# Kernel tuning notes

Measured on AMD Instinct MI355X. Metric: run time of the kernel, lower is better.

## Reference

```python
import jax, jax.numpy as jnp
import numpy as np

B, Cin, Cout, T, H, W = 8, 64, 64, 16, 32, 32
AH = 64  # attention_hidden_dims


def setup_inputs() -> dict:
    key = jax.random.key(0)
    ks = jax.random.split(key, 6)
    s = 0.05
    return {
        "X": jax.random.normal(ks[0], (B, Cin, T, H, W), jnp.float32),
        # 1x1 conv weights of the SelfAttention module (bias zero-init like nn.Conv2d default is uniform, but zeros is fine for a reference baseline)
        "q_w": jax.random.normal(ks[1], (AH, Cin), jnp.float32) * s,
        "q_b": jnp.zeros((AH,), jnp.float32),
        "k_w": jax.random.normal(ks[2], (AH, Cin), jnp.float32) * s,
        "k_b": jnp.zeros((AH,), jnp.float32),
        "v_w": jax.random.normal(ks[3], (Cin, Cin), jnp.float32) * s,
        "v_b": jnp.zeros((Cin,), jnp.float32),
        # ConvLSTM gate conv: concat([x, h]) -> 4*Cout channels, 3x3, padding 1
        "conv_w": jax.random.normal(ks[4], (4 * Cout, Cin + Cout, 3, 3), jnp.float32) * s,
        "conv_b": jnp.zeros((4 * Cout,), jnp.float32),
        # peephole weights, zero-init per WeightsInitializer.Zeros
        "w_ci": jnp.zeros((Cout, H, W), jnp.float32),
        "w_cf": jnp.zeros((Cout, H, W), jnp.float32),
        "w_co": jnp.zeros((Cout, H, W), jnp.float32),
    }


def _self_attention(x, q_w, q_b, k_w, k_b, v_w, v_b):
    # x: (B, Cin, H, W). 1x1 convs expressed as channel contractions.
    b, c, h, w = x.shape
    xf = x.reshape(b, c, h * w)                                    # (B, C, HW)
    q = jnp.einsum('oc,bcn->bno', q_w, xf) + q_b                   # (B, HW, AH)
    k = jnp.einsum('oc,bcn->bon', k_w, xf) + k_b[None, :, None]    # (B, AH, HW)
    v = jnp.einsum('oc,bcn->bon', v_w, xf) + v_b[None, :, None]    # (B, Cin, HW)
    attn = jax.nn.softmax(jnp.einsum('bno,bom->bnm', q, k), axis=-1)  # (B, HW, HW)
    out = jnp.einsum('bnm,bcm->bcn', attn, v).reshape(b, c, h, w)  # (B, Cin, H, W)
    return out, attn


def _convlstm_cell(x, h, c, conv_w, conv_b, w_ci, w_cf, w_co):
    z = jnp.concatenate([x, h], axis=1)  # (B, Cin+Cout, H, W)
    conv = jax.lax.conv_general_dilated(
        z, conv_w, window_strides=(1, 1), padding='SAME',
        dimension_numbers=('NCHW', 'OIHW', 'NCHW')) + conv_b[None, :, None, None]
    i_c, f_c, g_c, o_c = jnp.split(conv, 4, axis=1)
    i = jax.nn.sigmoid(i_c + w_ci * c)
    f = jax.nn.sigmoid(f_c + w_cf * c)
    new_c = f * c + i * jnp.tanh(g_c)
    o = jax.nn.sigmoid(o_c + w_co * new_c)
    new_h = o * jnp.tanh(new_c)
    return new_h, new_c


def reference(X, q_w, q_b, k_w, k_b, v_w, v_b, conv_w, conv_b, w_ci, w_cf, w_co):
    b = X.shape[0]
    h0 = jnp.zeros((b, Cout, H, W), X.dtype)
    c0 = jnp.zeros_like(h0)
    xs = jnp.moveaxis(X, 2, 0)  # (T, B, Cin, H, W) for scan over time

    def step(carry, x_t):
        h, c = carry
        ax, _ = _self_attention(x_t, q_w, q_b, k_w, k_b, v_w, v_b)
        new_h, new_c = _convlstm_cell(ax, h, c, conv_w, conv_b, w_ci, w_cf, w_co)
        return (new_h, new_c), new_h

    _, hs = jax.lax.scan(step, (h0, c0), xs)  # hs: (T, B, Cout, H, W)
    return jnp.moveaxis(hs, 0, 2)  # (B, Cout, T, H, W)
```

## Files before the change

### kernel.cpp

```cpp
#include <hip/hip_runtime.h>
#include <math.h>

typedef __attribute__((ext_vector_type(8))) __bf16 bf16x8;
typedef __attribute__((ext_vector_type(4))) float f32x4;
typedef unsigned short u16;
typedef unsigned int u32;

#define MFMA16(a, b, c) __builtin_amdgcn_mfma_f32_16x16x32_bf16(a, b, c, 0, 0, 0)

__device__ __forceinline__ u16 f2bf(float f) {
    u32 u = __float_as_uint(f);
    return (u16)((u + 0x7fffu + ((u >> 16) & 1u)) >> 16);
}
__device__ __forceinline__ float bf2f(u16 h) {
    return __uint_as_float(((u32)h) << 16);
}

__global__ __launch_bounds__(256) void k_wtrans2(const float* __restrict__ cw,
                                                 u16* __restrict__ whi,
                                                 u16* __restrict__ wlo) {
    int idx = blockIdx.x * 256 + threadIdx.x;
    if (idx >= 294912) return;
    int s   = idx >> 15;
    int ocp = (idx >> 7) & 255;
    int ic  = idx & 127;
    int q = ocp >> 5, cc = (ocp >> 2) & 7, g = ocp & 3;
    int oc = g * 64 + q * 8 + cc;
    float f = cw[oc * 1152 + ic * 9 + s];
    u16 hi = f2bf(f);
    whi[idx] = hi;
    wlo[idx] = f2bf(f - bf2f(hi));
}

__global__ __launch_bounds__(256) void k_qkvw(
    const float* __restrict__ qw, const float* __restrict__ kw,
    const float* __restrict__ vw, u16* __restrict__ w2h, u16* __restrict__ w2l)
{
    int idx = blockIdx.x * 256 + threadIdx.x;
    if (idx >= 12288) return;
    int o = idx >> 6, c = idx & 63;
    float f = (o < 64) ? qw[o * 64 + c]
            : (o < 128) ? kw[(o - 64) * 64 + c]
                        : vw[(o - 128) * 64 + c];
    u16 hi = f2bf(f);
    w2h[idx] = hi;
    w2l[idx] = f2bf(f - bf2f(hi));
}

__global__ __launch_bounds__(256) void k_qkv2(
    const float* __restrict__ X,
    const u16* __restrict__ w2h, const u16* __restrict__ w2l,
    const float* __restrict__ qb, const float* __restrict__ kb,
    const float* __restrict__ vb,
    u16* __restrict__ qmat, u16* __restrict__ kmat, u16* __restrict__ vt)
{
    __shared__ u16 bhs[4096];
    __shared__ u16 bls[4096];

    const int tid = threadIdx.x;
    const int ns = blockIdx.x;
    const int bt = blockIdx.y;
    const int b = bt >> 4, t = bt & 15;
    const int n0 = ns * 64;

    const float* xb = X + (size_t)b * 1048576 + (size_t)t * 1024 + n0;
    for (int i = tid; i < 4096; i += 256) {
        int c = i >> 6, n = i & 63;
        float f = xb[(size_t)c * 16384 + n];
        u16 hi = f2bf(f);
        u16 lo = f2bf(f - bf2f(hi));
        int ci = c ^ ((n & 7) << 3);
        bhs[n * 64 + ci] = hi;
        bls[n * 64 + ci] = lo;
    }
    __syncthreads();

    const int wv = tid >> 6, lane = tid & 63;
    const int l15 = lane & 15, l4 = lane >> 4;
    const int o0 = wv * 48;

    f32x4 acc[3][4];
#pragma unroll
    for (int ot = 0; ot < 3; ++ot)
#pragma unroll
        for (int nt = 0; nt < 4; ++nt) acc[ot][nt] = (f32x4){0.f, 0.f, 0.f, 0.f};

#pragma unroll
    for (int kk = 0; kk < 2; ++kk) {
        bf16x8 Ah[3], Al[3];
#pragma unroll
        for (int ot = 0; ot < 3; ++ot) {
            int off = (o0 + ot * 16 + l15) * 64 + kk * 32 + l4 * 8;
            Ah[ot] = *reinterpret_cast<const bf16x8*>(w2h + off);
            Al[ot] = *reinterpret_cast<const bf16x8*>(w2l + off);
        }
#pragma unroll
        for (int nt = 0; nt < 4; ++nt) {
            int n = nt * 16 + l15;
            int gran = (kk * 4 + l4) ^ (n & 7);
            bf16x8 Bh = *reinterpret_cast<const bf16x8*>(bhs + n * 64 + gran * 8);
            bf16x8 Bl = *reinterpret_cast<const bf16x8*>(bls + n * 64 + gran * 8);
#pragma unroll
            for (int ot = 0; ot < 3; ++ot) {
                acc[ot][nt] = MFMA16(Ah[ot], Bh, acc[ot][nt]);
                acc[ot][nt] = MFMA16(Ah[ot], Bl, acc[ot][nt]);
                acc[ot][nt] = MFMA16(Al[ot], Bh, acc[ot][nt]);
            }
        }
    }

#pragma unroll
    for (int ot = 0; ot < 3; ++ot) {
#pragma unroll
        for (int r = 0; r < 4; ++r) {
            int row = o0 + ot * 16 + l4 * 4 + r;
            float bias = (row < 64) ? qb[row]
                       : (row < 128) ? kb[row - 64] : vb[row - 128];
#pragma unroll
            for (int nt = 0; nt < 4; ++nt) {
                int col = n0 + nt * 16 + l15;
                u16 h = f2bf(acc[ot][nt][r] + bias);
                if (row < 64)
                    qmat[(size_t)bt * 65536 + (size_t)col * 64 + row] = h;
                else if (row < 128)
                    kmat[(size_t)bt * 65536 + (size_t)col * 64 + (row - 64)] = h;
                else
                    vt[(size_t)bt * 65536 + (size_t)(row - 128) * 1024 + col] = h;
            }
        }
    }
}

__global__ __launch_bounds__(256, 4) void k_attn(
    const u16* __restrict__ qmat, const u16* __restrict__ kmat,
    const u16* __restrict__ vt, u16* __restrict__ za)
{
    __shared__ char kl[16384];
    __shared__ char vl[16384];
    __shared__ u16 plds[4 * 16 * 40];

    const int tid = threadIdx.x;
    const int id  = blockIdx.x;
    const int w   = (id & 7) * 256 + (id >> 3);
    const int bt  = w >> 4;
    const int ntile = w & 15;

    const int wv = tid >> 6, lane = tid & 63;
    const int l15 = lane & 15, l4 = lane >> 4;
    const int n0 = ntile * 64 + wv * 16;

    const u16* qb_ = qmat + (size_t)bt * 65536;
    const u16* kb_ = kmat + (size_t)bt * 65536;
    const u16* vb_ = vt + (size_t)bt * 65536;

    bf16x8 qf0 = *reinterpret_cast<const bf16x8*>(qb_ + (n0 + l15) * 64 + l4 * 8);
    bf16x8 qf1 = *reinterpret_cast<const bf16x8*>(qb_ + (n0 + l15) * 64 + 32 + l4 * 8);

    f32x4 oacc[4];
#pragma unroll
    for (int ct = 0; ct < 4; ++ct) oacc[ct] = (f32x4){0.f, 0.f, 0.f, 0.f};
    float lsum = 0.f;
    char* plc = (char*)plds + wv * 1280;

    bf16x8 kst[4], vst[4];
#pragma unroll
    for (int r = 0; r < 4; ++r) {
        int c = tid + r * 256;
        kst[r] = *reinterpret_cast<const bf16x8*>(kb_ + (c >> 3) * 64 + (c & 7) * 8);
        vst[r] = *reinterpret_cast<const bf16x8*>(vb_ + (c >> 4) * 1024 + (c & 15) * 8);
    }

    for (int mt = 0; mt < 8; ++mt) {
        __syncthreads();
#pragma unroll
        for (int r = 0; r < 4; ++r) {
            int c = tid + r * 256;
            int m = c >> 3, sl = c & 7;
            *reinterpret_cast<bf16x8*>(kl + ((m * 128 + sl * 16) ^ ((m & 7) << 4))) = kst[r];
            int cc = c >> 4, sl2 = c & 15;
            *reinterpret_cast<bf16x8*>(vl + ((cc * 256 + sl2 * 16) ^ ((cc & 7) << 4))) = vst[r];
        }
        __syncthreads();
        if (mt < 7) {
            int mg = (mt + 1) * 128;
#pragma unroll
            for (int r = 0; r < 4; ++r) {
                int c = tid + r * 256;
                kst[r] = *reinterpret_cast<const bf16x8*>(kb_ + (mg + (c >> 3)) * 64 + (c & 7) * 8);
                vst[r] = *reinterpret_cast<const bf16x8*>(vb_ + (c >> 4) * 1024 + mg + (c & 15) * 8);
            }
        }

#pragma unroll
        for (int mi2 = 0; mi2 < 4; ++mi2) {
#pragma unroll
            for (int hf = 0; hf < 2; ++hf) {
                int ml = (mi2 * 2 + hf) * 16 + l15;
                f32x4 s = {0.f, 0.f, 0.f, 0.f};
                bf16x8 ka0 = *reinterpret_cast<const bf16x8*>(
                    kl + ((ml * 128 + l4 * 16) ^ ((ml & 7) << 4)));
                bf16x8 ka1 = *reinterpret_cast<const bf16x8*>(
                    kl + ((ml * 128 + 64 + l4 * 16) ^ ((ml & 7) << 4)));
                s = MFMA16(ka0, qf0, s);
                s = MFMA16(ka1, qf1, s);
                float p0 = __expf(s[0]);
                float p1 = __expf(s[1]);
                float p2 = __expf(s[2]);
                float p3 = __expf(s[3]);
                lsum += (p0 + p1) + (p2 + p3);
                u32 pa = (u32)f2bf(p0) | ((u32)f2bf(p1) << 16);
                u32 pb = (u32)f2bf(p2) | ((u32)f2bf(p3) << 16);
                *reinterpret_cast<uint2*>(plc + l15 * 80 + hf * 32 + l4 * 8) =
                    make_uint2(pa, pb);
            }
            bf16x8 pfrag = *reinterpret_cast<const bf16x8*>(plc + l15 * 80 + l4 * 16);
#pragma unroll
            for (int ct = 0; ct < 4; ++ct) {
                bf16x8 vfrag = *reinterpret_cast<const bf16x8*>(
                    vl + (((ct * 16 + l15) * 256 + mi2 * 64 + l4 * 16) ^ ((l15 & 7) << 4)));
                oacc[ct] = MFMA16(pfrag, vfrag, oacc[ct]);
            }
        }
    }

    lsum += __shfl_xor(lsum, 16, 64);
    lsum += __shfl_xor(lsum, 32, 64);

    u16* zab = za + (size_t)bt * 147968;
#pragma unroll
    for (int r = 0; r < 4; ++r) {
        float linv = 1.f / __shfl(lsum, l4 * 4 + r, 64);
        int nrow = n0 + l4 * 4 + r;
        u16* base = zab + (((nrow >> 5) + 1) * 34 + (nrow & 31) + 1) * 128;
#pragma unroll
        for (int ct = 0; ct < 4; ++ct) {
            float v = oacc[ct][r] * linv;
            u16 hi = f2bf(v);
            base[ct * 16 + l15]      = hi;
            base[64 + ct * 16 + l15] = f2bf(v - bf2f(hi));
        }
    }
}

__global__ __launch_bounds__(256) void k_cell3(
    const u16* __restrict__ za, const u16* __restrict__ zh_in,
    u16* __restrict__ zh_out, float* __restrict__ cst,
    const u16* __restrict__ whi, const u16* __restrict__ wlo,
    const float* __restrict__ conv_b,
    const float* __restrict__ wci, const float* __restrict__ wcf,
    const float* __restrict__ wco, float* __restrict__ out, int t)
{
    __shared__ __align__(16) char zt[26112];

    const int tid = threadIdx.x;
    const int id  = blockIdx.x;
    const int pxt = id & 63;
    const int oq  = id >> 6;
    const int b   = pxt >> 3;
    const int y0  = (pxt & 7) * 4;
    const int bt  = b * 16 + t;

    const int wv = tid >> 6, lane = tid & 63;
    const int l15 = lane & 15, l4 = lane >> 4;
    const int ow = wv & 1, pw = wv >> 1;

    const u16* zab = za + (size_t)bt * 147968;
    const u16* zhb = zh_in + (size_t)b * 147968;

    f32x4 acc[2][4];
#pragma unroll
    for (int sub = 0; sub < 2; ++sub)
#pragma unroll
        for (int nt = 0; nt < 4; ++nt) acc[sub][nt] = (f32x4){0.f, 0.f, 0.f, 0.f};

    for (int ck = 0; ck < 4; ++ck) {
        const u16* src = (ck < 2) ? zab : zhb;
        const int c0 = (ck & 1) * 32;
        __syncthreads();
        for (int g = tid; g < 1632; g += 256) {
            int p = g >> 3, slot = g & 7;
            int ly = p / 34, col = p - ly * 34;
            int gp = (y0 + ly) * 34 + col;
            int soff = (slot < 4) ? (c0 + slot * 8) : (64 + c0 + (slot - 4) * 8);
            uint4 v = *reinterpret_cast<const uint4*>(src + gp * 128 + soff);
            *reinterpret_cast<uint4*>(zt + p * 128 + ((slot * 16) ^ ((p & 7) << 4))) = v;
        }
        __syncthreads();

#pragma unroll
        for (int s = 0; s < 9; ++s) {
            const int dy = s / 3 - 1, dx = s % 3 - 1;
            bf16x8 Ah[2], Al[2];
#pragma unroll
            for (int sub = 0; sub < 2; ++sub) {
                size_t woff = (size_t)(s * 256 + oq * 64 + ow * 32 + sub * 16 + l15) * 128
                              + ck * 32 + l4 * 8;
                Ah[sub] = *reinterpret_cast<const bf16x8*>(whi + woff);
                Al[sub] = *reinterpret_cast<const bf16x8*>(wlo + woff);
            }
#pragma unroll
            for (int nt = 0; nt < 4; ++nt) {
                int pxl = (pw * 2 + (nt >> 1) + 1 + dy) * 34 + (nt & 1) * 16 + l15 + 1 + dx;
                int swz = (pxl & 7) << 4;
                bf16x8 Bh = *reinterpret_cast<const bf16x8*>(
                    zt + pxl * 128 + ((l4 * 16) ^ swz));
                bf16x8 Bl = *reinterpret_cast<const bf16x8*>(
                    zt + pxl * 128 + ((64 + l4 * 16) ^ swz));
#pragma unroll
                for (int sub = 0; sub < 2; ++sub) {
                    acc[sub][nt] = MFMA16(Ah[sub], Bh, acc[sub][nt]);
                    acc[sub][nt] = MFMA16(Ah[sub], Bl, acc[sub][nt]);
                    acc[sub][nt] = MFMA16(Al[sub], Bh, acc[sub][nt]);
                }
            }
        }
    }

    u16* zho = zh_out + (size_t)b * 147968;
    const int chq = (oq * 2 + ow) * 8;
#pragma unroll
    for (int sub = 0; sub < 2; ++sub) {
        int ch = chq + sub * 4 + l4;
        float bi = conv_b[ch], bf = conv_b[64 + ch];
        float bg = conv_b[128 + ch], bo = conv_b[192 + ch];
#pragma unroll
        for (int nt = 0; nt < 4; ++nt) {
            int y = y0 + pw * 2 + (nt >> 1);
            int x = (nt & 1) * 16 + l15;
            int n = y * 32 + x;
            float ci = acc[sub][nt][0] + bi;
            float cf = acc[sub][nt][1] + bf;
            float cg = acc[sub][nt][2] + bg;
            float co = acc[sub][nt][3] + bo;
            size_t si = ((size_t)b * 64 + ch) * 1024 + n;
            int pw_ = ch * 1024 + n;
            float cp = cst[si];
            float iv = 1.f / (1.f + __expf(-(ci + wci[pw_] * cp)));
            float fv = 1.f / (1.f + __expf(-(cf + wcf[pw_] * cp)));
            float nc = fv * cp + iv * tanhf(cg);
            float ov = 1.f / (1.f + __expf(-(co + wco[pw_] * nc)));
            float nh = ov * tanhf(nc);
            cst[si] = nc;
            out[(((size_t)b * 64 + ch) * 16 + t) * 1024 + n] = nh;
            u16 hhi = f2bf(nh);
            u16* zp = zho + ((y + 1) * 34 + (x + 1)) * 128;
            zp[ch]      = hhi;
            zp[64 + ch] = f2bf(nh - bf2f(hhi));
        }
    }
}

#define OB_Q    0ull
#define OB_K    16777216ull
#define OB_V    33554432ull
#define OB_ZA   50331648ull
#define OB_ZH0  88211456ull
#define OB_ZH1  90578944ull
#define OB_CST  92946432ull
#define OB_WHI  95043584ull
#define OB_WLO  95633408ull
#define OB_WQ2H 96223232ull
#define OB_WQ2L 96247808ull

extern "C" void kernel_launch(void* const* d_in, const int* in_sizes, int n_in,
                              void* d_out, int out_size, void* d_ws, size_t ws_size,
                              hipStream_t stream)
{
    const float* X   = (const float*)d_in[0];
    const float* qw  = (const float*)d_in[1];
    const float* qb  = (const float*)d_in[2];
    const float* kw  = (const float*)d_in[3];
    const float* kb  = (const float*)d_in[4];
    const float* vw  = (const float*)d_in[5];
    const float* vb  = (const float*)d_in[6];
    const float* cw  = (const float*)d_in[7];
    const float* cb  = (const float*)d_in[8];
    const float* wci = (const float*)d_in[9];
    const float* wcf = (const float*)d_in[10];
    const float* wco = (const float*)d_in[11];
    float* out = (float*)d_out;
    char* wsb  = (char*)d_ws;

    u16* qmat = (u16*)(wsb + OB_Q);
    u16* kmat = (u16*)(wsb + OB_K);
    u16* vt   = (u16*)(wsb + OB_V);
    u16* za   = (u16*)(wsb + OB_ZA);
    u16* zh0  = (u16*)(wsb + OB_ZH0);
    u16* zh1  = (u16*)(wsb + OB_ZH1);
    float* cst= (float*)(wsb + OB_CST);
    u16* whi  = (u16*)(wsb + OB_WHI);
    u16* wlo  = (u16*)(wsb + OB_WLO);
    u16* w2h  = (u16*)(wsb + OB_WQ2H);
    u16* w2l  = (u16*)(wsb + OB_WQ2L);

    hipMemsetAsync(za, 0, 37879808ull, stream);
    hipMemsetAsync(zh0, 0, 6832128ull, stream);
    k_wtrans2<<<1152, 256, 0, stream>>>(cw, whi, wlo);
    k_qkvw<<<48, 256, 0, stream>>>(qw, kw, vw, w2h, w2l);
    k_qkv2<<<dim3(16, 128), 256, 0, stream>>>(X, w2h, w2l, qb, kb, vb,
                                              qmat, kmat, vt);
    k_attn<<<2048, 256, 0, stream>>>(qmat, kmat, vt, za);

    for (int t = 0; t < 16; ++t) {
        u16* hin  = (t & 1) ? zh1 : zh0;
        u16* hout = (t & 1) ? zh0 : zh1;
        k_cell3<<<256, 256, 0, stream>>>(za, hin, hout, cst, whi, wlo,
                                         cb, wci, wcf, wco, out, t);
    }
}
```

Before: 620.1 us.

## Widen attention blocks, zero za halo in-kernel, split cell grid finer

The attention kernel now uses 512-thread blocks covering 128 query rows, so each staged K/V tile is shared by twice as many waves. One block per batch-time also zeroes only the padded halo of za, which replaces the full 37 MB memset. The ConvLSTM cell kernel processes 2 rows per block instead of 4 and launches 512 blocks, with the block index swizzled. This gives more parallelism for the sequential per-timestep launches, at the cost of more redundant halo loads relative to useful work.

```diff
diff --git a/kernel.cpp b/kernel.cpp
--- a/kernel.cpp
+++ b/kernel.cpp
@@ -131,27 +131,39 @@
     }
 }
 
-__global__ __launch_bounds__(256, 4) void k_attn(
+__global__ __launch_bounds__(512, 2) void k_attn2(
     const u16* __restrict__ qmat, const u16* __restrict__ kmat,
     const u16* __restrict__ vt, u16* __restrict__ za)
 {
     __shared__ char kl[16384];
     __shared__ char vl[16384];
-    __shared__ u16 plds[4 * 16 * 40];
+    __shared__ u16 plds[8 * 16 * 40];
 
     const int tid = threadIdx.x;
     const int id  = blockIdx.x;
-    const int w   = (id & 7) * 256 + (id >> 3);
-    const int bt  = w >> 4;
-    const int ntile = w & 15;
+    const int w   = (id & 7) * 128 + (id >> 3);
+    const int bt  = w >> 3;
+    const int nt8 = w & 7;
 
     const int wv = tid >> 6, lane = tid & 63;
     const int l15 = lane & 15, l4 = lane >> 4;
-    const int n0 = ntile * 64 + wv * 16;
+    const int n0 = nt8 * 128 + wv * 16;
 
     const u16* qb_ = qmat + (size_t)bt * 65536;
     const u16* kb_ = kmat + (size_t)bt * 65536;
     const u16* vb_ = vt + (size_t)bt * 65536;
+    u16* zab = za + (size_t)bt * 147968;
+
+    if (nt8 == 0) {
+        for (int j = tid; j < 2112; j += 512) {
+            int pi = j >> 4, q16 = j & 15;
+            int px = (pi < 34) ? pi
+                   : (pi < 68) ? (33 * 34 + (pi - 34))
+                               : ((1 + ((pi - 68) >> 1)) * 34 + ((pi - 68) & 1) * 33);
+            *reinterpret_cast<uint4*>(zab + px * 128 + q16 * 8) =
+                make_uint4(0u, 0u, 0u, 0u);
+        }
+    }
 
     bf16x8 qf0 = *reinterpret_cast<const bf16x8*>(qb_ + (n0 + l15) * 64 + l4 * 8);
     bf16x8 qf1 = *reinterpret_cast<const bf16x8*>(qb_ + (n0 + l15) * 64 + 32 + l4 * 8);
@@ -162,10 +174,10 @@
     float lsum = 0.f;
     char* plc = (char*)plds + wv * 1280;
 
-    bf16x8 kst[4], vst[4];
-#pragma unroll
-    for (int r = 0; r < 4; ++r) {
-        int c = tid + r * 256;
+    bf16x8 kst[2], vst[2];
+#pragma unroll
+    for (int r = 0; r < 2; ++r) {
+        int c = tid + r * 512;
         kst[r] = *reinterpret_cast<const bf16x8*>(kb_ + (c >> 3) * 64 + (c & 7) * 8);
         vst[r] = *reinterpret_cast<const bf16x8*>(vb_ + (c >> 4) * 1024 + (c & 15) * 8);
     }
@@ -173,8 +185,8 @@
     for (int mt = 0; mt < 8; ++mt) {
         __syncthreads();
 #pragma unroll
-        for (int r = 0; r < 4; ++r) {
-            int c = tid + r * 256;
+        for (int r = 0; r < 2; ++r) {
+            int c = tid + r * 512;
             int m = c >> 3, sl = c & 7;
             *reinterpret_cast<bf16x8*>(kl + ((m * 128 + sl * 16) ^ ((m & 7) << 4))) = kst[r];
             int cc = c >> 4, sl2 = c & 15;
@@ -184,8 +196,8 @@
         if (mt < 7) {
             int mg = (mt + 1) * 128;
 #pragma unroll
-            for (int r = 0; r < 4; ++r) {
-                int c = tid + r * 256;
+            for (int r = 0; r < 2; ++r) {
+                int c = tid + r * 512;
                 kst[r] = *reinterpret_cast<const bf16x8*>(kb_ + (mg + (c >> 3)) * 64 + (c & 7) * 8);
                 vst[r] = *reinterpret_cast<const bf16x8*>(vb_ + (c >> 4) * 1024 + mg + (c & 15) * 8);
             }
@@ -226,7 +238,6 @@
     lsum += __shfl_xor(lsum, 16, 64);
     lsum += __shfl_xor(lsum, 32, 64);
 
-    u16* zab = za + (size_t)bt * 147968;
 #pragma unroll
     for (int r = 0; r < 4; ++r) {
         float linv = 1.f / __shfl(lsum, l4 * 4 + r, 64);
@@ -242,7 +253,7 @@
     }
 }
 
-__global__ __launch_bounds__(256) void k_cell3(
+__global__ __launch_bounds__(256) void k_cell4(
     const u16* __restrict__ za, const u16* __restrict__ zh_in,
     u16* __restrict__ zh_out, float* __restrict__ cst,
     const u16* __restrict__ whi, const u16* __restrict__ wlo,
@@ -250,14 +261,15 @@
     const float* __restrict__ wci, const float* __restrict__ wcf,
     const float* __restrict__ wco, float* __restrict__ out, int t)
 {
-    __shared__ __align__(16) char zt[26112];
+    __shared__ __align__(16) char zt[17408];
 
     const int tid = threadIdx.x;
     const int id  = blockIdx.x;
-    const int pxt = id & 63;
-    const int oq  = id >> 6;
-    const int b   = pxt >> 3;
-    const int y0  = (pxt & 7) * 4;
+    const int w   = (id & 7) * 64 + (id >> 3);
+    const int b   = w >> 6;
+    const int oq  = (w >> 4) & 3;
+    const int ys  = w & 15;
+    const int y0  = ys * 2;
     const int bt  = b * 16 + t;
 
     const int wv = tid >> 6, lane = tid & 63;
@@ -267,17 +279,17 @@
     const u16* zab = za + (size_t)bt * 147968;
     const u16* zhb = zh_in + (size_t)b * 147968;
 
-    f32x4 acc[2][4];
+    f32x4 acc[2][2];
 #pragma unroll
     for (int sub = 0; sub < 2; ++sub)
 #pragma unroll
-        for (int nt = 0; nt < 4; ++nt) acc[sub][nt] = (f32x4){0.f, 0.f, 0.f, 0.f};
+        for (int nt = 0; nt < 2; ++nt) acc[sub][nt] = (f32x4){0.f, 0.f, 0.f, 0.f};
 
     for (int ck = 0; ck < 4; ++ck) {
         const u16* src = (ck < 2) ? zab : zhb;
         const int c0 = (ck & 1) * 32;
         __syncthreads();
-        for (int g = tid; g < 1632; g += 256) {
+        for (int g = tid; g < 1088; g += 256) {
             int p = g >> 3, slot = g & 7;
             int ly = p / 34, col = p - ly * 34;
             int gp = (y0 + ly) * 34 + col;
@@ -299,8 +311,8 @@
                 Al[sub] = *reinterpret_cast<const bf16x8*>(wlo + woff);
             }
 #pragma unroll
-            for (int nt = 0; nt < 4; ++nt) {
-                int pxl = (pw * 2 + (nt >> 1) + 1 + dy) * 34 + (nt & 1) * 16 + l15 + 1 + dx;
+            for (int nt = 0; nt < 2; ++nt) {
+                int pxl = (pw + dy + 1) * 34 + nt * 16 + l15 + 1 + dx;
                 int swz = (pxl & 7) << 4;
                 bf16x8 Bh = *reinterpret_cast<const bf16x8*>(
                     zt + pxl * 128 + ((l4 * 16) ^ swz));
@@ -318,15 +330,15 @@
 
     u16* zho = zh_out + (size_t)b * 147968;
     const int chq = (oq * 2 + ow) * 8;
+    const int y = y0 + pw;
 #pragma unroll
     for (int sub = 0; sub < 2; ++sub) {
         int ch = chq + sub * 4 + l4;
         float bi = conv_b[ch], bf = conv_b[64 + ch];
         float bg = conv_b[128 + ch], bo = conv_b[192 + ch];
 #pragma unroll
-        for (int nt = 0; nt < 4; ++nt) {
-            int y = y0 + pw * 2 + (nt >> 1);
-            int x = (nt & 1) * 16 + l15;
+        for (int nt = 0; nt < 2; ++nt) {
+            int x = nt * 16 + l15;
             int n = y * 32 + x;
             float ci = acc[sub][nt][0] + bi;
             float cf = acc[sub][nt][1] + bf;
@@ -393,18 +405,17 @@
     u16* w2h  = (u16*)(wsb + OB_WQ2H);
     u16* w2l  = (u16*)(wsb + OB_WQ2L);
 
-    hipMemsetAsync(za, 0, 37879808ull, stream);
     hipMemsetAsync(zh0, 0, 6832128ull, stream);
     k_wtrans2<<<1152, 256, 0, stream>>>(cw, whi, wlo);
     k_qkvw<<<48, 256, 0, stream>>>(qw, kw, vw, w2h, w2l);
     k_qkv2<<<dim3(16, 128), 256, 0, stream>>>(X, w2h, w2l, qb, kb, vb,
                                               qmat, kmat, vt);
-    k_attn<<<2048, 256, 0, stream>>>(qmat, kmat, vt, za);
+    k_attn2<<<1024, 512, 0, stream>>>(qmat, kmat, vt, za);
 
     for (int t = 0; t < 16; ++t) {
         u16* hin  = (t & 1) ? zh1 : zh0;
         u16* hout = (t & 1) ? zh0 : zh1;
-        k_cell3<<<256, 256, 0, stream>>>(za, hin, hout, cst, whi, wlo,
+        k_cell4<<<512, 256, 0, stream>>>(za, hin, hout, cst, whi, wlo,
                                          cb, wci, wcf, wco, out, t);
     }
 }
```

Measured after the change: 740.1 us. 19.4% more time.
